# Kernel tuning notes

Measured on AMD Instinct MI355X. Metric: run time of the kernel, lower is better.

The kernel has to match this reference:

```python
import jax, jax.numpy as jnp
import numpy as np
from jax import lax

B, L, H, K = 256, 512, 768, 64


def setup_inputs() -> dict:
    key = jax.random.key(0)
    k1, k2, k3, k4, k5 = jax.random.split(key, 5)
    features = jax.random.normal(k1, (B, L, H), dtype=jnp.float32)
    W = jax.random.normal(k2, (H, K), dtype=jnp.float32) * 0.02
    b = jnp.zeros((K,), dtype=jnp.float32)
    transition = jax.random.normal(k3, (K, K), dtype=jnp.float32)
    tags = jax.random.randint(k4, (B, L), 0, K, dtype=jnp.int64)
    # variable sentence lengths in decreasing order (repo sorts batches by length)
    lengths = jnp.sort(jax.random.randint(k5, (B,), L // 4, L + 1))[::-1]
    mask = jnp.arange(L)[None, :] < lengths[:, None]  # (B, L) bool, pads at end
    return {"features": features, "W": W, "b": b, "transition": transition,
            "tags": tags, "mask": mask}


def reference(features, W, b, transition, tags, mask):
    # encode: hidden2tag linear (dropout is identity in eval)
    emit = jnp.einsum("blh,hk->blk", features, W) + b  # (B, L, K)
    maskf = mask.astype(emit.dtype)

    # gold path score
    gold_emit = jnp.take_along_axis(emit, tags[:, :, None], axis=2)[..., 0]  # (B, L)
    trans_sc = transition[tags[:, :-1], tags[:, 1:]]                          # (B, L-1)
    score = gold_emit.at[:, 1:].add(trans_sc)
    total_score = (score * maskf).sum(axis=1)                                 # (B,)

    # CRF forward algorithm (log partition) via scan over time
    d0 = emit[:, 0]  # (B, K)
    emit_t = jnp.moveaxis(emit[:, 1:], 1, 0)  # (L-1, B, K)
    mask_t = mask[:, 1:].T                    # (L-1, B)

    def step(d, xs):
        e_t, m_t = xs
        # log_sum[b, j, k] = d[b, j] + transition[j, k] + e_t[b, k]
        log_sum = d[:, :, None] + transition[None, :, :] + e_t[:, None, :]
        d_new = jax.scipy.special.logsumexp(log_sum, axis=1)  # (B, K)
        d = jnp.where(m_t[:, None], d_new, d)  # finished sequences keep old d
        return d, None

    d, _ = lax.scan(step, d0, (emit_t, mask_t))
    log_z = jax.scipy.special.logsumexp(d, axis=1)  # (B,)

    return log_z - total_score  # negative log-likelihood per sentence, (B,)
```

## Files before the change

### kernel.cpp

```cpp
#include <hip/hip_runtime.h>
#include <hip/hip_bf16.h>
#include <string.h>

#define B_ 256
#define L_ 512
#define H_ 768
#define K_ 64
#define WT_OFF 33554432

typedef float  float4v  __attribute__((ext_vector_type(4)));
typedef float  float2v  __attribute__((ext_vector_type(2)));
typedef short  short8v  __attribute__((ext_vector_type(8)));

union BFragU { uint4 u4; short8v s8; };

__device__ inline unsigned short f2bf_bits(float f) {
    union { float f; unsigned int u; } c; c.f = f;
    unsigned int u = c.u;
    u += 0x7fffu + ((u >> 16) & 1u);
    return (unsigned short)(u >> 16);
}

__device__ inline float2v mk2(float x, float y) { float2v v; v.x = x; v.y = y; return v; }

__global__ void wt_transpose(const float* __restrict__ W, unsigned int* __restrict__ Wt) {
    int k = blockIdx.x;
    int j = threadIdx.x;
    float a = W[(size_t)(2 * j) * K_ + k];
    float b = W[(size_t)(2 * j + 1) * K_ + k];
    unsigned int u = (unsigned int)f2bf_bits(a) | ((unsigned int)f2bf_bits(b) << 16);
    Wt[k * (H_ / 2) + j] = u;
}

template<int NC>
struct Stage {
    uint4  b[4];
    float4 a[NC][2];
};

template<int NC>
__device__ __forceinline__ void load_stage(Stage<NC>& s, const float* __restrict__ A,
        const unsigned short* __restrict__ Wt, int rowbase, int ks, int lm, int lq) {
    #pragma unroll
    for (int nt = 0; nt < 4; ++nt)
        s.b[nt] = *reinterpret_cast<const uint4*>(
            Wt + (size_t)(lm + nt * 16) * H_ + ks * 32 + lq * 8);
    #pragma unroll
    for (int c = 0; c < NC; ++c) {
        const float* ap = A + (size_t)(rowbase + c * 64) * H_ + ks * 32 + lq * 8;
        s.a[c][0] = *reinterpret_cast<const float4*>(ap);
        s.a[c][1] = *reinterpret_cast<const float4*>(ap + 4);
    }
}

template<int NC>
__device__ __forceinline__ void consume_stage(const Stage<NC>& s, float4v acc[][4]) {
    short8v bfrag[4];
    #pragma unroll
    for (int nt = 0; nt < 4; ++nt) { BFragU u; u.u4 = s.b[nt]; bfrag[nt] = u.s8; }
    #pragma unroll
    for (int c = 0; c < NC; ++c) {
        __hip_bfloat162 tt[4];
        tt[0] = __float22bfloat162_rn(make_float2(s.a[c][0].x, s.a[c][0].y));
        tt[1] = __float22bfloat162_rn(make_float2(s.a[c][0].z, s.a[c][0].w));
        tt[2] = __float22bfloat162_rn(make_float2(s.a[c][1].x, s.a[c][1].y));
        tt[3] = __float22bfloat162_rn(make_float2(s.a[c][1].z, s.a[c][1].w));
        short8v afrag;
        memcpy(&afrag, tt, 16);
        #pragma unroll
        for (int nt = 0; nt < 4; ++nt)
            acc[c][nt] = __builtin_amdgcn_mfma_f32_16x16x32_bf16(
                afrag, bfrag[nt], acc[c][nt], 0, 0, 0);
    }
}

template<int NC>
__device__ __forceinline__ void gemm_body(const float* __restrict__ A,
        const unsigned short* __restrict__ Wt, const float* __restrict__ bias,
        float* __restrict__ emit, int blk, int tid) {
    const int lane = tid & 63;
    const int wid  = tid >> 6;
    const int lm   = lane & 15;
    const int lq   = lane >> 4;
    const int rowbase = blk * 128 + wid * 16 + lm;

    float4v acc[NC][4];
    #pragma unroll
    for (int c = 0; c < NC; ++c)
        #pragma unroll
        for (int nt = 0; nt < 4; ++nt)
            acc[c][nt] = (float4v)0.f;

    Stage<NC> s0, s1;
    load_stage<NC>(s0, A, Wt, rowbase, 0, lm, lq);
    #pragma unroll 1
    for (int ks = 0; ks < 24; ks += 2) {
        load_stage<NC>(s1, A, Wt, rowbase, ks + 1, lm, lq);
        consume_stage<NC>(s0, acc);
        load_stage<NC>(s0, A, Wt, rowbase, (ks + 2 < 24) ? ks + 2 : 23, lm, lq);
        consume_stage<NC>(s1, acc);
    }

    float bv[4];
    #pragma unroll
    for (int nt = 0; nt < 4; ++nt) bv[nt] = bias[nt * 16 + lm];
    #pragma unroll
    for (int c = 0; c < NC; ++c) {
        int rowb = blk * 128 + c * 64 + wid * 16 + lq * 4;
        #pragma unroll
        for (int nt = 0; nt < 4; ++nt) {
            int col = nt * 16 + lm;
            #pragma unroll
            for (int r = 0; r < 4; ++r)
                emit[(size_t)(rowb + r) * K_ + col] = acc[c][nt][r] + bv[nt];
        }
    }
}

__global__ __launch_bounds__(256, 2)
void emit_gemm(const float* __restrict__ A, const unsigned short* __restrict__ Wt,
               const float* __restrict__ bias, const int* __restrict__ mask,
               float* __restrict__ emit) {
    const int r0 = blockIdx.x * 128;
    if (mask[r0] == 0) return;
    if (mask[r0 + 64])
        gemm_body<2>(A, Wt, bias, emit, blockIdx.x, threadIdx.x);
    else
        gemm_body<1>(A, Wt, bias, emit, blockIdx.x, threadIdx.x);
}

__global__ __launch_bounds__(64, 1)
void crf_scan(const float* __restrict__ emit, const float* __restrict__ T,
              const int* __restrict__ tags, const int* __restrict__ mask,
              float* __restrict__ out) {
    const int b    = blockIdx.x;
    const int lane = threadIdx.x;
    __shared__ __align__(16) float ebuf[2][16 * 64];
    __shared__ __align__(16) float qbuf[2][64];

    int len = 0;
    #pragma unroll
    for (int j = 0; j < 8; ++j) len += (mask[b * L_ + j * 64 + lane] != 0);
    #pragma unroll
    for (int off = 32; off; off >>= 1) len += __shfl_xor(len, off, 64);

    float2v et2[32];
    #pragma unroll
    for (int j = 0; j < 32; ++j) {
        et2[j].x = __expf(T[(2 * j) * K_ + lane]);
        et2[j].y = __expf(T[(2 * j + 1) * K_ + lane]);
    }

    const float* eb = emit + (size_t)b * L_ * K_;

    float sc = 0.f;
    for (int t = lane; t < len; t += 64) {
        int tg = tags[b * L_ + t];
        sc += eb[(size_t)t * K_ + tg];
        if (t > 0) sc += T[tags[b * L_ + t - 1] * K_ + tg];
    }
    #pragma unroll
    for (int off = 32; off; off >>= 1) sc += __shfl_xor(sc, off, 64);

    float e00 = eb[lane];
    float M = __int_as_float(__builtin_amdgcn_readfirstlane(__float_as_int(e00)));
    float q = __expf(e00 - M);
    qbuf[0][lane] = q;
    int prev_eps = 0;

    const int soff = ((lane >> 2) << 6) + ((lane & 3) << 4);
    {
        const float4* src = reinterpret_cast<const float4*>(eb + soff);
        float4 r0 = src[0], r1 = src[1], r2 = src[2], r3 = src[3];
        float4* dst = reinterpret_cast<float4*>(&ebuf[0][soff]);
        dst[0] = r0; dst[1] = r1; dst[2] = r2; dst[3] = r3;
    }

    int cur = 0;
    int t = 1;
    for (int c = 0;; ++c) {
        const int nt0  = (c + 1) << 4;
        const bool more = nt0 < len;
        float4 r0, r1, r2, r3;
        if (more) {
            const float4* src = reinterpret_cast<const float4*>(eb + nt0 * K_ + soff);
            r0 = src[0]; r1 = src[1]; r2 = src[2]; r3 = src[3];
        }
        const int tend = more ? nt0 : len;
        for (; t < tend; ++t) {
            float e  = ebuf[cur][((t & 15) << 6) + lane];
            float ef = __int_as_float(__builtin_amdgcn_readfirstlane(__float_as_int(e)));
            float delta = (float)prev_eps * 0.69314718f + ef;
            M += delta;
            float f = __expf(e - delta);

            const float4* qb4 = reinterpret_cast<const float4*>(&qbuf[(t + 1) & 1][0]);
            float2v a0 = mk2(0.f, 0.f), a1 = mk2(0.f, 0.f);
            float2v a2 = mk2(0.f, 0.f), a3 = mk2(0.f, 0.f);
            #pragma unroll
            for (int r = 0; r < 16; r += 2) {
                float4 p0 = qb4[r];
                float4 p1 = qb4[r + 1];
                a0 += mk2(p0.x, p0.y) * et2[2 * r];
                a1 += mk2(p0.z, p0.w) * et2[2 * r + 1];
                a2 += mk2(p1.x, p1.y) * et2[2 * r + 2];
                a3 += mk2(p1.z, p1.w) * et2[2 * r + 3];
            }
            float2v s2 = (a0 + a1) + (a2 + a3);
            float s = s2.x + s2.y;
            unsigned su = (unsigned)__builtin_amdgcn_readfirstlane(__float_as_int(s));
            prev_eps = (int)((su >> 23) & 0xff) - 127;
            q = s * f;
            qbuf[t & 1][lane] = q;
        }
        if (!more) break;
        float4* dst = reinterpret_cast<float4*>(&ebuf[cur ^ 1][soff]);
        dst[0] = r0; dst[1] = r1; dst[2] = r2; dst[3] = r3;
        cur ^= 1;
    }

    float z = q;
    #pragma unroll
    for (int off = 32; off; off >>= 1) z += __shfl_xor(z, off, 64);
    if (lane == 0) out[b] = M + __logf(z) - sc;
}

extern "C" void kernel_launch(void* const* d_in, const int* in_sizes, int n_in,
                              void* d_out, int out_size, void* d_ws, size_t ws_size,
                              hipStream_t stream) {
    const float* feat = (const float*)d_in[0];
    const float* W    = (const float*)d_in[1];
    const float* bias = (const float*)d_in[2];
    const float* T    = (const float*)d_in[3];
    const int*   tags = (const int*)d_in[4];
    const int*   mask = (const int*)d_in[5];
    float* out  = (float*)d_out;
    float* emit = (float*)d_ws;
    unsigned int*   WtW = (unsigned int*)((char*)d_ws + WT_OFF);
    unsigned short* Wt  = (unsigned short*)WtW;

    hipLaunchKernelGGL(wt_transpose, dim3(K_),   dim3(H_ / 2), 0, stream, W, WtW);
    hipLaunchKernelGGL(emit_gemm,    dim3(1024), dim3(256),    0, stream, feat, Wt, bias, mask, emit);
    hipLaunchKernelGGL(crf_scan,     dim3(B_),   dim3(64),     0, stream, emit, T, tags, mask, out);
}
```

Measured before the change: 730.2 us.

## Split GEMM into per-wave 64-row blocks and register-prefetch CRF emissions

The emission GEMM now gives each block 64 rows (one 16-row tile per wave) with a per-wave mask early-exit, doubling the grid and raising the occupancy hint to 3 blocks per CU. This is meant to balance load and skip padded rows more finely. The CRF scan drops the LDS double-buffered emission staging and instead keeps an 8-deep rotating register prefetch of emission rows loaded straight from global memory, which removes the LDS round trip. The risk is that global load latency now sits directly in the serial recurrence, with only eight steps of prefetch to hide it.

```diff
diff --git a/kernel.cpp b/kernel.cpp
--- a/kernel.cpp
+++ b/kernel.cpp
@@ -32,101 +32,76 @@
     Wt[k * (H_ / 2) + j] = u;
 }
 
-template<int NC>
-struct Stage {
+struct StageS {
     uint4  b[4];
-    float4 a[NC][2];
+    float4 a[2];
 };
 
-template<int NC>
-__device__ __forceinline__ void load_stage(Stage<NC>& s, const float* __restrict__ A,
+__device__ __forceinline__ void load_stageS(StageS& s, const float* __restrict__ A,
         const unsigned short* __restrict__ Wt, int rowbase, int ks, int lm, int lq) {
     #pragma unroll
     for (int nt = 0; nt < 4; ++nt)
         s.b[nt] = *reinterpret_cast<const uint4*>(
             Wt + (size_t)(lm + nt * 16) * H_ + ks * 32 + lq * 8);
-    #pragma unroll
-    for (int c = 0; c < NC; ++c) {
-        const float* ap = A + (size_t)(rowbase + c * 64) * H_ + ks * 32 + lq * 8;
-        s.a[c][0] = *reinterpret_cast<const float4*>(ap);
-        s.a[c][1] = *reinterpret_cast<const float4*>(ap + 4);
-    }
-}
-
-template<int NC>
-__device__ __forceinline__ void consume_stage(const Stage<NC>& s, float4v acc[][4]) {
+    const float* ap = A + (size_t)rowbase * H_ + ks * 32 + lq * 8;
+    s.a[0] = *reinterpret_cast<const float4*>(ap);
+    s.a[1] = *reinterpret_cast<const float4*>(ap + 4);
+}
+
+__device__ __forceinline__ void consume_stageS(const StageS& s, float4v acc[4]) {
     short8v bfrag[4];
     #pragma unroll
     for (int nt = 0; nt < 4; ++nt) { BFragU u; u.u4 = s.b[nt]; bfrag[nt] = u.s8; }
-    #pragma unroll
-    for (int c = 0; c < NC; ++c) {
-        __hip_bfloat162 tt[4];
-        tt[0] = __float22bfloat162_rn(make_float2(s.a[c][0].x, s.a[c][0].y));
-        tt[1] = __float22bfloat162_rn(make_float2(s.a[c][0].z, s.a[c][0].w));
-        tt[2] = __float22bfloat162_rn(make_float2(s.a[c][1].x, s.a[c][1].y));
-        tt[3] = __float22bfloat162_rn(make_float2(s.a[c][1].z, s.a[c][1].w));
-        short8v afrag;
-        memcpy(&afrag, tt, 16);
-        #pragma unroll
-        for (int nt = 0; nt < 4; ++nt)
-            acc[c][nt] = __builtin_amdgcn_mfma_f32_16x16x32_bf16(
-                afrag, bfrag[nt], acc[c][nt], 0, 0, 0);
-    }
-}
-
-template<int NC>
-__device__ __forceinline__ void gemm_body(const float* __restrict__ A,
-        const unsigned short* __restrict__ Wt, const float* __restrict__ bias,
-        float* __restrict__ emit, int blk, int tid) {
+    __hip_bfloat162 tt[4];
+    tt[0] = __float22bfloat162_rn(make_float2(s.a[0].x, s.a[0].y));
+    tt[1] = __float22bfloat162_rn(make_float2(s.a[0].z, s.a[0].w));
+    tt[2] = __float22bfloat162_rn(make_float2(s.a[1].x, s.a[1].y));
+    tt[3] = __float22bfloat162_rn(make_float2(s.a[1].z, s.a[1].w));
+    short8v afrag;
+    memcpy(&afrag, tt, 16);
+    #pragma unroll
+    for (int nt = 0; nt < 4; ++nt)
+        acc[nt] = __builtin_amdgcn_mfma_f32_16x16x32_bf16(afrag, bfrag[nt], acc[nt], 0, 0, 0);
+}
+
+__global__ __launch_bounds__(256, 3)
+void emit_gemm(const float* __restrict__ A, const unsigned short* __restrict__ Wt,
+               const float* __restrict__ bias, const int* __restrict__ mask,
+               float* __restrict__ emit) {
+    const int tid  = threadIdx.x;
     const int lane = tid & 63;
     const int wid  = tid >> 6;
     const int lm   = lane & 15;
     const int lq   = lane >> 4;
-    const int rowbase = blk * 128 + wid * 16 + lm;
-
-    float4v acc[NC][4];
-    #pragma unroll
-    for (int c = 0; c < NC; ++c)
-        #pragma unroll
-        for (int nt = 0; nt < 4; ++nt)
-            acc[c][nt] = (float4v)0.f;
-
-    Stage<NC> s0, s1;
-    load_stage<NC>(s0, A, Wt, rowbase, 0, lm, lq);
+    const int r0   = blockIdx.x * 64;
+    if (mask[r0 + wid * 16] == 0) return;
+    const int rowbase = r0 + wid * 16 + lm;
+
+    float4v acc[4];
+    #pragma unroll
+    for (int nt = 0; nt < 4; ++nt) acc[nt] = (float4v)0.f;
+
+    StageS s0, s1;
+    load_stageS(s0, A, Wt, rowbase, 0, lm, lq);
     #pragma unroll 1
     for (int ks = 0; ks < 24; ks += 2) {
-        load_stage<NC>(s1, A, Wt, rowbase, ks + 1, lm, lq);
-        consume_stage<NC>(s0, acc);
-        load_stage<NC>(s0, A, Wt, rowbase, (ks + 2 < 24) ? ks + 2 : 23, lm, lq);
-        consume_stage<NC>(s1, acc);
+        load_stageS(s1, A, Wt, rowbase, ks + 1, lm, lq);
+        consume_stageS(s0, acc);
+        load_stageS(s0, A, Wt, rowbase, (ks + 2 < 24) ? ks + 2 : 23, lm, lq);
+        consume_stageS(s1, acc);
     }
 
     float bv[4];
     #pragma unroll
     for (int nt = 0; nt < 4; ++nt) bv[nt] = bias[nt * 16 + lm];
-    #pragma unroll
-    for (int c = 0; c < NC; ++c) {
-        int rowb = blk * 128 + c * 64 + wid * 16 + lq * 4;
+    const int rowb = r0 + wid * 16 + lq * 4;
+    #pragma unroll
+    for (int nt = 0; nt < 4; ++nt) {
+        int col = nt * 16 + lm;
         #pragma unroll
-        for (int nt = 0; nt < 4; ++nt) {
-            int col = nt * 16 + lm;
-            #pragma unroll
-            for (int r = 0; r < 4; ++r)
-                emit[(size_t)(rowb + r) * K_ + col] = acc[c][nt][r] + bv[nt];
-        }
-    }
-}
-
-__global__ __launch_bounds__(256, 2)
-void emit_gemm(const float* __restrict__ A, const unsigned short* __restrict__ Wt,
-               const float* __restrict__ bias, const int* __restrict__ mask,
-               float* __restrict__ emit) {
-    const int r0 = blockIdx.x * 128;
-    if (mask[r0] == 0) return;
-    if (mask[r0 + 64])
-        gemm_body<2>(A, Wt, bias, emit, blockIdx.x, threadIdx.x);
-    else
-        gemm_body<1>(A, Wt, bias, emit, blockIdx.x, threadIdx.x);
+        for (int r = 0; r < 4; ++r)
+            emit[(size_t)(rowb + r) * K_ + col] = acc[nt][r] + bv[nt];
+    }
 }
 
 __global__ __launch_bounds__(64, 1)
@@ -135,7 +110,6 @@
               float* __restrict__ out) {
     const int b    = blockIdx.x;
     const int lane = threadIdx.x;
-    __shared__ __align__(16) float ebuf[2][16 * 64];
     __shared__ __align__(16) float qbuf[2][64];
 
     int len = 0;
@@ -154,10 +128,10 @@
     const float* eb = emit + (size_t)b * L_ * K_;
 
     float sc = 0.f;
-    for (int t = lane; t < len; t += 64) {
-        int tg = tags[b * L_ + t];
-        sc += eb[(size_t)t * K_ + tg];
-        if (t > 0) sc += T[tags[b * L_ + t - 1] * K_ + tg];
+    for (int tt = lane; tt < len; tt += 64) {
+        int tg = tags[b * L_ + tt];
+        sc += eb[(size_t)tt * K_ + tg];
+        if (tt > 0) sc += T[tags[b * L_ + tt - 1] * K_ + tg];
     }
     #pragma unroll
     for (int off = 32; off; off >>= 1) sc += __shfl_xor(sc, off, 64);
@@ -166,57 +140,57 @@
     float M = __int_as_float(__builtin_amdgcn_readfirstlane(__float_as_int(e00)));
     float q = __expf(e00 - M);
     qbuf[0][lane] = q;
-    int prev_eps = 0;
-
-    const int soff = ((lane >> 2) << 6) + ((lane & 3) << 4);
-    {
-        const float4* src = reinterpret_cast<const float4*>(eb + soff);
-        float4 r0 = src[0], r1 = src[1], r2 = src[2], r3 = src[3];
-        float4* dst = reinterpret_cast<float4*>(&ebuf[0][soff]);
-        dst[0] = r0; dst[1] = r1; dst[2] = r2; dst[3] = r3;
-    }
-
-    int cur = 0;
+
+    float eA[4], eB[4];
+    #pragma unroll
+    for (int i = 0; i < 4; ++i) {
+        eA[i] = eb[(size_t)(1 + i) * K_ + lane];
+        eB[i] = eb[(size_t)(5 + i) * K_ + lane];
+    }
+
+    int eps = 0;
     int t = 1;
-    for (int c = 0;; ++c) {
-        const int nt0  = (c + 1) << 4;
-        const bool more = nt0 < len;
-        float4 r0, r1, r2, r3;
-        if (more) {
-            const float4* src = reinterpret_cast<const float4*>(eb + nt0 * K_ + soff);
-            r0 = src[0]; r1 = src[1]; r2 = src[2]; r3 = src[3];
+
+    auto step = [&](float& ereg) {
+        float e = ereg;
+        int tp = t + 8; if (tp > L_ - 1) tp = L_ - 1;
+        ereg = eb[(size_t)tp * K_ + lane];
+        float ef = __int_as_float(__builtin_amdgcn_readfirstlane(__float_as_int(e)));
+        float delta = (float)eps * 0.69314718f + ef;
+        M += delta;
+        float f = __expf(e - delta);
+
+        const float4* qb4 = reinterpret_cast<const float4*>(&qbuf[(t + 1) & 1][0]);
+        float2v a0 = mk2(0.f, 0.f), a1 = mk2(0.f, 0.f);
+        float2v a2 = mk2(0.f, 0.f), a3 = mk2(0.f, 0.f);
+        #pragma unroll
+        for (int r = 0; r < 16; r += 2) {
+            float4 p0 = qb4[r];
+            float4 p1 = qb4[r + 1];
+            a0 += mk2(p0.x, p0.y) * et2[2 * r];
+            a1 += mk2(p0.z, p0.w) * et2[2 * r + 1];
+            a2 += mk2(p1.x, p1.y) * et2[2 * r + 2];
+            a3 += mk2(p1.z, p1.w) * et2[2 * r + 3];
         }
-        const int tend = more ? nt0 : len;
-        for (; t < tend; ++t) {
-            float e  = ebuf[cur][((t & 15) << 6) + lane];
-            float ef = __int_as_float(__builtin_amdgcn_readfirstlane(__float_as_int(e)));
-            float delta = (float)prev_eps * 0.69314718f + ef;
-            M += delta;
-            float f = __expf(e - delta);
-
-            const float4* qb4 = reinterpret_cast<const float4*>(&qbuf[(t + 1) & 1][0]);
-            float2v a0 = mk2(0.f, 0.f), a1 = mk2(0.f, 0.f);
-            float2v a2 = mk2(0.f, 0.f), a3 = mk2(0.f, 0.f);
-            #pragma unroll
-            for (int r = 0; r < 16; r += 2) {
-                float4 p0 = qb4[r];
-                float4 p1 = qb4[r + 1];
-                a0 += mk2(p0.x, p0.y) * et2[2 * r];
-                a1 += mk2(p0.z, p0.w) * et2[2 * r + 1];
-                a2 += mk2(p1.x, p1.y) * et2[2 * r + 2];
-                a3 += mk2(p1.z, p1.w) * et2[2 * r + 3];
-            }
-            float2v s2 = (a0 + a1) + (a2 + a3);
-            float s = s2.x + s2.y;
-            unsigned su = (unsigned)__builtin_amdgcn_readfirstlane(__float_as_int(s));
-            prev_eps = (int)((su >> 23) & 0xff) - 127;
-            q = s * f;
-            qbuf[t & 1][lane] = q;
-        }
-        if (!more) break;
-        float4* dst = reinterpret_cast<float4*>(&ebuf[cur ^ 1][soff]);
-        dst[0] = r0; dst[1] = r1; dst[2] = r2; dst[3] = r3;
-        cur ^= 1;
+        float2v s2 = (a0 + a1) + (a2 + a3);
+        float s = s2.x + s2.y;
+        unsigned su = (unsigned)__builtin_amdgcn_readfirstlane(__float_as_int(s));
+        eps = (int)((su >> 23) & 0xffu) - 127;
+        q = s * f;
+        qbuf[t & 1][lane] = q;
+        ++t;
+    };
+
+    #pragma unroll 1
+    while (t < len) {
+        step(eA[0]); if (t >= len) break;
+        step(eA[1]); if (t >= len) break;
+        step(eA[2]); if (t >= len) break;
+        step(eA[3]); if (t >= len) break;
+        step(eB[0]); if (t >= len) break;
+        step(eB[1]); if (t >= len) break;
+        step(eB[2]); if (t >= len) break;
+        step(eB[3]);
     }
 
     float z = q;
@@ -240,6 +214,6 @@
     unsigned short* Wt  = (unsigned short*)WtW;
 
     hipLaunchKernelGGL(wt_transpose, dim3(K_),   dim3(H_ / 2), 0, stream, W, WtW);
-    hipLaunchKernelGGL(emit_gemm,    dim3(1024), dim3(256),    0, stream, feat, Wt, bias, mask, emit);
+    hipLaunchKernelGGL(emit_gemm,    dim3(2048), dim3(256),    0, stream, feat, Wt, bias, mask, emit);
     hipLaunchKernelGGL(crf_scan,     dim3(B_),   dim3(64),     0, stream, emit, T, tags, mask, out);
 }
```

After: 705.7 us. 1.03x faster.
